# Kernel tuning notes

Measured on AMD Instinct MI355X. Metric: run time of the kernel, lower is better.

## Reference

```python
import jax, jax.numpy as jnp
import numpy as np

HEAD = 12
HEAD_DIM = 64  # dim // head = 768 // 12


def setup_inputs() -> dict:
    key = jax.random.key(0)
    k1, k2, k3 = jax.random.split(key, 3)
    B, N, D = 4, 2048, 768
    scale = 1.0 / np.sqrt(D)
    return {
        "x": jax.random.normal(k1, (B, N, D), dtype=jnp.float32),
        "w_qkv": jax.random.normal(k2, (D, 3 * D), dtype=jnp.float32) * scale,
        "w_proj": jax.random.normal(k3, (D, D), dtype=jnp.float32) * scale,
        "b_proj": jnp.zeros((D,), dtype=jnp.float32),
    }


def reference(x, w_qkv, w_proj, b_proj):
    B, N, D = x.shape
    qkv = x @ w_qkv  # [B, N, 3D]
    q, k, v = jnp.split(qkv, 3, axis=-1)
    # [B, H, N, k]
    def heads(t):
        return t.reshape(B, N, HEAD, HEAD_DIM).transpose(0, 2, 1, 3)
    q, k, v = heads(q), heads(k), heads(v)
    attn = jnp.einsum("bhnd,bhmd->bhnm", q, k) / jnp.sqrt(jnp.float32(HEAD_DIM))
    attn_prob = jax.nn.softmax(attn, axis=-1)  # dropout p=0.0 -> identity
    out = jnp.einsum("bhnm,bhmd->bhnd", attn_prob, v)
    out = out.transpose(0, 2, 1, 3).reshape(B, N, D)
    return out @ w_proj + b_proj
```

## Files before the change

### kernel.cpp

```cpp
#include <hip/hip_runtime.h>

typedef unsigned short u16;
typedef unsigned int u32;
typedef u16 u16x4 __attribute__((ext_vector_type(4)));
typedef u16 u16x8 __attribute__((ext_vector_type(8)));
typedef u32 u32x4 __attribute__((ext_vector_type(4)));
typedef __bf16 bf16x8 __attribute__((ext_vector_type(8)));
typedef float f32x4 __attribute__((ext_vector_type(4)));
typedef float f32x16 __attribute__((ext_vector_type(16)));

#define MFMA16 __builtin_amdgcn_mfma_f32_16x16x32_bf16
#define MFMA32 __builtin_amdgcn_mfma_f32_32x32x16_bf16

__device__ __forceinline__ u16 f2bf(float f) {
  return __builtin_bit_cast(u16, (__bf16)f);
}

__device__ __forceinline__ u32 pk2bf(float a, float b) {
  return (u32)__builtin_bit_cast(u16, (__bf16)a) |
         ((u32)__builtin_bit_cast(u16, (__bf16)b) << 16);
}

__device__ __forceinline__ void gload_lds16(const void* g, void* l) {
  __builtin_amdgcn_global_load_lds(
      (const __attribute__((address_space(1))) u32*)g,
      (__attribute__((address_space(3))) u32*)l, 16, 0, 0);
}

__global__ void cvt_f32_bf16_kernel(const float* __restrict__ in,
                                    u16* __restrict__ out, int n4) {
  int i = blockIdx.x * blockDim.x + threadIdx.x;
  if (i >= n4) return;
  float4 v = reinterpret_cast<const float4*>(in)[i];
  u16x4 o;
  o[0] = f2bf(v.x); o[1] = f2bf(v.y); o[2] = f2bf(v.z); o[3] = f2bf(v.w);
  reinterpret_cast<u16x4*>(out)[i] = o;
}

__global__ void transpose_cvt_kernel(const float* __restrict__ w,
                                     u16* __restrict__ wt, int K, int N) {
  __shared__ float t[32][33];
  int bk = blockIdx.x * 32, bn = blockIdx.y * 32;
  int x = threadIdx.x, y = threadIdx.y;
#pragma unroll
  for (int j = 0; j < 32; j += 8)
    t[y + j][x] = w[(size_t)(bk + y + j) * N + bn + x];
  __syncthreads();
#pragma unroll
  for (int j = 0; j < 32; j += 8)
    wt[(size_t)(bn + y + j) * K + bk + x] = f2bf(t[x][y + j]);
}

#define QSCALE 0.18033688011112042f

template <int NTOT, int EPI>
__global__ __launch_bounds__(256)
void gemm_bf16_kernel(const u16* __restrict__ A, const u16* __restrict__ BT,
                      u16* __restrict__ qo, u16* __restrict__ ko,
                      u16* __restrict__ vt, float* __restrict__ outF,
                      const float* __restrict__ bias) {
  __shared__ u16 sh[16384];
  u16* As = sh;
  u16* Bs = sh + 8192;
  const int tid = threadIdx.x;
  const int l = tid & 63, w = tid >> 6;
  const int lr = l & 15, lg = l >> 4;
  const int mtile = blockIdx.x & 63;
  const int ntile = blockIdx.x >> 6;
  const int mbase = mtile * 128, nbase = ntile * 128;
  const int wr = (w >> 1) * 64, wc = (w & 1) * 64;

  f32x4 acc[4][4] = {};

  for (int k0 = 0; k0 < 768; k0 += 64) {
#pragma unroll
    for (int i = 0; i < 4; ++i) {
      const int c = w * 64 + i * 256 + l;
      const int row = c >> 3, c16 = c & 7;
      const int sc = c16 ^ (row & 7);
      gload_lds16(A + (size_t)(mbase + row) * 768 + k0 + sc * 8,
                  &As[(size_t)(w * 64 + i * 256) * 8]);
      gload_lds16(BT + (size_t)(nbase + row) * 768 + k0 + sc * 8,
                  &Bs[(size_t)(w * 64 + i * 256) * 8]);
    }
    __syncthreads();
#pragma unroll
    for (int ks = 0; ks < 2; ++ks) {
      bf16x8 af[4], bfr[4];
#pragma unroll
      for (int m = 0; m < 4; ++m) {
        const int row = wr + m * 16 + lr;
        const int byte = (row * 128 + ks * 64 + lg * 16) ^ ((row & 7) << 4);
        af[m] = *reinterpret_cast<const bf16x8*>((const char*)As + byte);
      }
#pragma unroll
      for (int n = 0; n < 4; ++n) {
        const int row = wc + n * 16 + lr;
        const int byte = (row * 128 + ks * 64 + lg * 16) ^ ((row & 7) << 4);
        bfr[n] = *reinterpret_cast<const bf16x8*>((const char*)Bs + byte);
      }
#pragma unroll
      for (int m = 0; m < 4; ++m)
#pragma unroll
        for (int n = 0; n < 4; ++n)
          acc[m][n] = MFMA16(af[m], bfr[n], acc[m][n], 0, 0, 0);
    }
    __syncthreads();
  }

  if (EPI == 0 && ntile >= 12) {
    u16* vts = sh;
#pragma unroll
    for (int m = 0; m < 4; ++m)
#pragma unroll
      for (int n = 0; n < 4; ++n)
#pragma unroll
        for (int r = 0; r < 4; ++r) {
          const int col = wc + n * 16 + lr;
          const int row = wr + m * 16 + lg * 4 + r;
          const int byte = col * 256 + ((row * 2) ^ ((col & 7) << 4));
          *reinterpret_cast<u16*>((char*)vts + byte) = f2bf(acc[m][n][r]);
        }
    __syncthreads();
    const int b2 = mbase >> 11, nn0 = mbase & 2047;
#pragma unroll
    for (int i = 0; i < 8; ++i) {
      const int idx = i * 256 + tid;
      const int col = idx >> 4, u = idx & 15;
      u16x8 vv = *reinterpret_cast<u16x8*>(
          (char*)vts + (col * 256 + ((u * 16) ^ ((col & 7) << 4))));
      const int cg = nbase - 1536 + col;
      const int hh = cg >> 6, dd = cg & 63;
      *reinterpret_cast<u16x8*>(
          vt + (((size_t)(b2 * 12 + hh)) * 64 + dd) * 2048 + nn0 + u * 8) = vv;
    }
    return;
  }

#pragma unroll
  for (int m = 0; m < 4; ++m) {
#pragma unroll
    for (int n = 0; n < 4; ++n) {
#pragma unroll
      for (int r = 0; r < 4; ++r) {
        const int row = mbase + wr + m * 16 + lg * 4 + r;
        const int col = nbase + wc + n * 16 + lr;
        float val = acc[m][n][r];
        if (EPI == 0) {
          const int w2 = col / 768;
          const int c2 = col - w2 * 768;
          const int hh = c2 >> 6, dd = c2 & 63;
          const int b2 = row >> 11, nn = row & 2047;
          u16* dst = (w2 == 0) ? qo : ko;
          if (w2 == 0) val *= QSCALE;
          dst[(((size_t)(b2 * 12 + hh)) * 2048 + nn) * 64 + dd] = f2bf(val);
        } else {
          outF[(size_t)row * NTOT + col] = val + bias[col];
        }
      }
    }
  }
}

__global__ __launch_bounds__(256)
void flash_attn32_kernel(const u16* __restrict__ qb, const u16* __restrict__ kb,
                         const u16* __restrict__ vtb, u16* __restrict__ ao) {
  __shared__ u16 sh[16384];
  const int tid = threadIdx.x, w = tid >> 6, l = tid & 63;
  const int q5 = l & 31, hi = l >> 5;
  const int swz = (blockIdx.x & 7) * 96 + (blockIdx.x >> 3);
  const int bh = swz >> 4, qt = swz & 15;
  const int b = bh / 12, h = bh % 12;
  const int qrow0 = qt * 128 + w * 32;
  const u16* Q = qb + ((size_t)bh * 2048 + qrow0) * 64;
  const u16* K = kb + (size_t)bh * 2048 * 64;
  const u16* Vg = vtb + (size_t)bh * 64 * 2048;

  bf16x8 qf[4];
#pragma unroll
  for (int dk = 0; dk < 4; ++dk)
    qf[dk] = *reinterpret_cast<const bf16x8*>(Q + (size_t)q5 * 64 + dk * 16 + hi * 8);

  f32x16 ot0 = {}, ot1 = {};
  float l_ = 0.f;

  auto stage = [&](u16* base, int kt) {
#pragma unroll
    for (int i = 0; i < 2; ++i) {
      const int c = w * 64 + i * 256 + l;
      const int row = c >> 3, sc = (c & 7) ^ (row & 7);
      gload_lds16(K + (size_t)(kt + row) * 64 + sc * 8,
                  base + (size_t)(w * 64 + i * 256) * 8);
    }
#pragma unroll
    for (int i = 0; i < 2; ++i) {
      const int c = w * 64 + i * 256 + l;
      const int row = c >> 3, sc = (c & 7) ^ (row & 7);
      gload_lds16(Vg + (size_t)row * 2048 + kt + sc * 8,
                  base + 4096 + (size_t)(w * 64 + i * 256) * 8);
    }
  };

  stage(sh, 0);
  int cur = 0;
  const int swq = (q5 & 7) << 4;

  for (int kt = 0; kt < 2048; kt += 64) {
    u16* tb = sh + cur * 8192;
    __builtin_amdgcn_sched_barrier(0);
    __builtin_amdgcn_s_barrier();
    __builtin_amdgcn_sched_barrier(0);
    if (kt + 64 < 2048) {
      stage(sh + (cur ^ 1) * 8192, kt + 64);
      asm volatile("s_waitcnt vmcnt(4)" ::: "memory");
    } else {
      asm volatile("s_waitcnt vmcnt(0)" ::: "memory");
    }
    __builtin_amdgcn_sched_barrier(0);
    __builtin_amdgcn_s_barrier();
    __builtin_amdgcn_sched_barrier(0);

    const char* ksb = (const char*)tb;
    const char* vsb = (const char*)(tb + 4096);

    f32x16 st0 = {}, st1 = {};
    __builtin_amdgcn_s_setprio(1);
#pragma unroll
    for (int dk = 0; dk < 4; ++dk) {
      const int off = dk * 32 + hi * 16;
      bf16x8 kf0 = *reinterpret_cast<const bf16x8*>(ksb + ((q5 * 128 + off) ^ swq));
      bf16x8 kf1 = *reinterpret_cast<const bf16x8*>(ksb + (((q5 + 32) * 128 + off) ^ swq));
      st0 = MFMA32(kf0, qf[dk], st0, 0, 0, 0);
      st1 = MFMA32(kf1, qf[dk], st1, 0, 0, 0);
    }
    __builtin_amdgcn_s_setprio(0);

    float ls = 0.f;
#pragma unroll
    for (int r = 0; r < 16; ++r) {
      st0[r] = __builtin_amdgcn_exp2f(st0[r]); ls += st0[r];
    }
#pragma unroll
    for (int r = 0; r < 16; ++r) {
      st1[r] = __builtin_amdgcn_exp2f(st1[r]); ls += st1[r];
    }
    l_ += ls + __shfl_xor(ls, 32);

    __builtin_amdgcn_s_setprio(1);
#pragma unroll
    for (int kvs = 0; kvs < 4; ++kvs) {
      const f32x16& stx = (kvs < 2) ? st0 : st1;
      const int rb = (kvs & 1) * 8;
      const u32 A0 = pk2bf(stx[rb + 0], stx[rb + 1]);
      const u32 A1 = pk2bf(stx[rb + 2], stx[rb + 3]);
      const u32 A2 = pk2bf(stx[rb + 4], stx[rb + 5]);
      const u32 A3 = pk2bf(stx[rb + 6], stx[rb + 7]);
      const u32 s1 = hi ? A0 : A2, s2 = hi ? A1 : A3;
      const u32 r1 = (u32)__shfl_xor((int)s1, 32);
      const u32 r2 = (u32)__shfl_xor((int)s2, 32);
      u32x4 wv;
      wv[0] = hi ? r1 : A0; wv[1] = hi ? r2 : A1;
      wv[2] = hi ? A2 : r1; wv[3] = hi ? A3 : r2;
      const bf16x8 pf = __builtin_bit_cast(bf16x8, wv);
      const int off = kvs * 32 + hi * 16;
      bf16x8 vf0 = *reinterpret_cast<const bf16x8*>(vsb + ((q5 * 128 + off) ^ swq));
      bf16x8 vf1 = *reinterpret_cast<const bf16x8*>(vsb + (((q5 + 32) * 128 + off) ^ swq));
      ot0 = MFMA32(vf0, pf, ot0, 0, 0, 0);
      ot1 = MFMA32(vf1, pf, ot1, 0, 0, 0);
    }
    __builtin_amdgcn_s_setprio(0);
    cur ^= 1;
  }

  u16* ob = sh + w * 2048;
  const float inv = 1.0f / l_;
#pragma unroll
  for (int g = 0; g < 4; ++g) {
    u16x4 pk0, pk1;
#pragma unroll
    for (int r = 0; r < 4; ++r) {
      pk0[r] = f2bf(ot0[g * 4 + r] * inv);
      pk1[r] = f2bf(ot1[g * 4 + r] * inv);
    }
    const int d0 = hi * 4 + g * 8;
    *reinterpret_cast<u16x4*>((char*)ob + ((q5 * 128 + d0 * 2) ^ swq)) = pk0;
    *reinterpret_cast<u16x4*>((char*)ob + ((q5 * 128 + (d0 + 32) * 2) ^ swq)) = pk1;
  }
  __syncthreads();
#pragma unroll
  for (int i = 0; i < 4; ++i) {
    const int idx = i * 64 + l;
    const int qr = idx >> 3, cc = idx & 7;
    u16x8 vv = *reinterpret_cast<u16x8*>(
        (char*)ob + ((qr * 128 + cc * 16) ^ ((qr & 7) << 4)));
    *reinterpret_cast<u16x8*>(
        ao + ((size_t)(b * 2048 + qrow0 + qr)) * 768 + h * 64 + cc * 8) = vv;
  }
}

extern "C" void kernel_launch(void* const* d_in, const int* in_sizes, int n_in,
                              void* d_out, int out_size, void* d_ws,
                              size_t ws_size, hipStream_t stream) {
  const float* x = (const float*)d_in[0];
  const float* w_qkv = (const float*)d_in[1];
  const float* w_proj = (const float*)d_in[2];
  const float* b_proj = (const float*)d_in[3];
  float* out = (float*)d_out;

  char* ws = (char*)d_ws;
  size_t off = 0;
  auto alloc = [&](size_t bytes) {
    char* p = ws + off;
    off += (bytes + 255) & ~(size_t)255;
    return p;
  };
  u16* xb = (u16*)alloc(8192ull * 768 * 2);
  u16* wqkvT = (u16*)alloc(2304ull * 768 * 2);
  u16* wprojT = (u16*)alloc(768ull * 768 * 2);
  u16* qbuf = (u16*)alloc(48ull * 2048 * 64 * 2);
  u16* kbuf = (u16*)alloc(48ull * 2048 * 64 * 2);
  u16* vtb = (u16*)alloc(48ull * 64 * 2048 * 2);
  u16* aob = (u16*)alloc(8192ull * 768 * 2);
  (void)ws_size; (void)n_in; (void)in_sizes; (void)out_size;

  cvt_f32_bf16_kernel<<<(8192 * 768 / 4) / 256, 256, 0, stream>>>(
      x, xb, 8192 * 768 / 4);
  transpose_cvt_kernel<<<dim3(768 / 32, 2304 / 32), dim3(32, 8), 0, stream>>>(
      w_qkv, wqkvT, 768, 2304);
  transpose_cvt_kernel<<<dim3(768 / 32, 768 / 32), dim3(32, 8), 0, stream>>>(
      w_proj, wprojT, 768, 768);

  gemm_bf16_kernel<2304, 0><<<64 * 18, 256, 0, stream>>>(
      xb, wqkvT, qbuf, kbuf, vtb, nullptr, nullptr);

  flash_attn32_kernel<<<768, 256, 0, stream>>>(qbuf, kbuf, vtb, aob);

  gemm_bf16_kernel<768, 1><<<64 * 6, 256, 0, stream>>>(
      aob, wprojT, nullptr, nullptr, nullptr, out, b_proj);
}
```

Measured before the change: 164.3 us.

## Stage two KV tiles per barrier window and use permlane32 swap

The flash attention loop now loads two 64-key K/V tiles per pipeline stage into a doubled shared buffer, which halves the number of barrier pairs per block and deepens prefetch. The P-matrix lane exchange now uses the permlane32_swap builtin when it is available, in place of two ds_bpermute shuffles plus selects. The cost is double the LDS per block (64KB), which may lower occupancy.

Result: faster. 158.8 us (-3.3%).

```diff
diff --git a/kernel.cpp b/kernel.cpp
--- a/kernel.cpp
+++ b/kernel.cpp
@@ -4,6 +4,7 @@
 typedef unsigned int u32;
 typedef u16 u16x4 __attribute__((ext_vector_type(4)));
 typedef u16 u16x8 __attribute__((ext_vector_type(8)));
+typedef u32 u32x2 __attribute__((ext_vector_type(2)));
 typedef u32 u32x4 __attribute__((ext_vector_type(4)));
 typedef __bf16 bf16x8 __attribute__((ext_vector_type(8)));
 typedef float f32x4 __attribute__((ext_vector_type(4)));
@@ -19,6 +20,19 @@
 __device__ __forceinline__ u32 pk2bf(float a, float b) {
   return (u32)__builtin_bit_cast(u16, (__bf16)a) |
          ((u32)__builtin_bit_cast(u16, (__bf16)b) << 16);
+}
+
+__device__ __forceinline__ u32x2 swap32(u32 a, u32 b, int hi) {
+#if __has_builtin(__builtin_amdgcn_permlane32_swap)
+  (void)hi;
+  return __builtin_amdgcn_permlane32_swap(a, b, false, false);
+#else
+  u32 sa = (u32)__shfl_xor((int)a, 32), sb = (u32)__shfl_xor((int)b, 32);
+  u32x2 r;
+  r[0] = hi ? sb : a;
+  r[1] = hi ? b : sa;
+  return r;
+#endif
 }
 
 __device__ __forceinline__ void gload_lds16(const void* g, void* l) {
@@ -165,7 +179,7 @@
 __global__ __launch_bounds__(256)
 void flash_attn32_kernel(const u16* __restrict__ qb, const u16* __restrict__ kb,
                          const u16* __restrict__ vtb, u16* __restrict__ ao) {
-  __shared__ u16 sh[16384];
+  __shared__ u16 sh[32768];
   const int tid = threadIdx.x, w = tid >> 6, l = tid & 63;
   const int q5 = l & 31, hi = l >> 5;
   const int swz = (blockIdx.x & 7) * 96 + (blockIdx.x >> 3);
@@ -184,35 +198,40 @@
   f32x16 ot0 = {}, ot1 = {};
   float l_ = 0.f;
 
-  auto stage = [&](u16* base, int kt) {
-#pragma unroll
-    for (int i = 0; i < 2; ++i) {
-      const int c = w * 64 + i * 256 + l;
-      const int row = c >> 3, sc = (c & 7) ^ (row & 7);
-      gload_lds16(K + (size_t)(kt + row) * 64 + sc * 8,
-                  base + (size_t)(w * 64 + i * 256) * 8);
-    }
-#pragma unroll
-    for (int i = 0; i < 2; ++i) {
-      const int c = w * 64 + i * 256 + l;
-      const int row = c >> 3, sc = (c & 7) ^ (row & 7);
-      gload_lds16(Vg + (size_t)row * 2048 + kt + sc * 8,
-                  base + 4096 + (size_t)(w * 64 + i * 256) * 8);
+  auto stage2 = [&](u16* base, int kt0) {
+#pragma unroll
+    for (int s = 0; s < 2; ++s) {
+      u16* sb = base + s * 8192;
+      const int kt = kt0 + s * 64;
+#pragma unroll
+      for (int i = 0; i < 2; ++i) {
+        const int c = w * 64 + i * 256 + l;
+        const int row = c >> 3, sc = (c & 7) ^ (row & 7);
+        gload_lds16(K + (size_t)(kt + row) * 64 + sc * 8,
+                    sb + (size_t)(w * 64 + i * 256) * 8);
+      }
+#pragma unroll
+      for (int i = 0; i < 2; ++i) {
+        const int c = w * 64 + i * 256 + l;
+        const int row = c >> 3, sc = (c & 7) ^ (row & 7);
+        gload_lds16(Vg + (size_t)row * 2048 + kt + sc * 8,
+                    sb + 4096 + (size_t)(w * 64 + i * 256) * 8);
+      }
     }
   };
 
-  stage(sh, 0);
+  stage2(sh, 0);
   int cur = 0;
   const int swq = (q5 & 7) << 4;
 
-  for (int kt = 0; kt < 2048; kt += 64) {
-    u16* tb = sh + cur * 8192;
+  for (int win = 0; win < 16; ++win) {
+    u16* tb = sh + cur * 16384;
     __builtin_amdgcn_sched_barrier(0);
     __builtin_amdgcn_s_barrier();
     __builtin_amdgcn_sched_barrier(0);
-    if (kt + 64 < 2048) {
-      stage(sh + (cur ^ 1) * 8192, kt + 64);
-      asm volatile("s_waitcnt vmcnt(4)" ::: "memory");
+    if (win + 1 < 16) {
+      stage2(sh + (cur ^ 1) * 16384, (win + 1) * 128);
+      asm volatile("s_waitcnt vmcnt(8)" ::: "memory");
     } else {
       asm volatile("s_waitcnt vmcnt(0)" ::: "memory");
     }
@@ -220,55 +239,55 @@
     __builtin_amdgcn_s_barrier();
     __builtin_amdgcn_sched_barrier(0);
 
-    const char* ksb = (const char*)tb;
-    const char* vsb = (const char*)(tb + 4096);
-
-    f32x16 st0 = {}, st1 = {};
-    __builtin_amdgcn_s_setprio(1);
-#pragma unroll
-    for (int dk = 0; dk < 4; ++dk) {
-      const int off = dk * 32 + hi * 16;
-      bf16x8 kf0 = *reinterpret_cast<const bf16x8*>(ksb + ((q5 * 128 + off) ^ swq));
-      bf16x8 kf1 = *reinterpret_cast<const bf16x8*>(ksb + (((q5 + 32) * 128 + off) ^ swq));
-      st0 = MFMA32(kf0, qf[dk], st0, 0, 0, 0);
-      st1 = MFMA32(kf1, qf[dk], st1, 0, 0, 0);
-    }
-    __builtin_amdgcn_s_setprio(0);
-
-    float ls = 0.f;
-#pragma unroll
-    for (int r = 0; r < 16; ++r) {
-      st0[r] = __builtin_amdgcn_exp2f(st0[r]); ls += st0[r];
-    }
-#pragma unroll
-    for (int r = 0; r < 16; ++r) {
-      st1[r] = __builtin_amdgcn_exp2f(st1[r]); ls += st1[r];
-    }
-    l_ += ls + __shfl_xor(ls, 32);
-
-    __builtin_amdgcn_s_setprio(1);
-#pragma unroll
-    for (int kvs = 0; kvs < 4; ++kvs) {
-      const f32x16& stx = (kvs < 2) ? st0 : st1;
-      const int rb = (kvs & 1) * 8;
-      const u32 A0 = pk2bf(stx[rb + 0], stx[rb + 1]);
-      const u32 A1 = pk2bf(stx[rb + 2], stx[rb + 3]);
-      const u32 A2 = pk2bf(stx[rb + 4], stx[rb + 5]);
-      const u32 A3 = pk2bf(stx[rb + 6], stx[rb + 7]);
-      const u32 s1 = hi ? A0 : A2, s2 = hi ? A1 : A3;
-      const u32 r1 = (u32)__shfl_xor((int)s1, 32);
-      const u32 r2 = (u32)__shfl_xor((int)s2, 32);
-      u32x4 wv;
-      wv[0] = hi ? r1 : A0; wv[1] = hi ? r2 : A1;
-      wv[2] = hi ? A2 : r1; wv[3] = hi ? A3 : r2;
-      const bf16x8 pf = __builtin_bit_cast(bf16x8, wv);
-      const int off = kvs * 32 + hi * 16;
-      bf16x8 vf0 = *reinterpret_cast<const bf16x8*>(vsb + ((q5 * 128 + off) ^ swq));
-      bf16x8 vf1 = *reinterpret_cast<const bf16x8*>(vsb + (((q5 + 32) * 128 + off) ^ swq));
-      ot0 = MFMA32(vf0, pf, ot0, 0, 0, 0);
-      ot1 = MFMA32(vf1, pf, ot1, 0, 0, 0);
-    }
-    __builtin_amdgcn_s_setprio(0);
+    for (int s = 0; s < 2; ++s) {
+      const char* ksb = (const char*)(tb + s * 8192);
+      const char* vsb = (const char*)(tb + s * 8192 + 4096);
+
+      f32x16 st0 = {}, st1 = {};
+      __builtin_amdgcn_s_setprio(1);
+#pragma unroll
+      for (int dk = 0; dk < 4; ++dk) {
+        const int off = dk * 32 + hi * 16;
+        bf16x8 kf0 = *reinterpret_cast<const bf16x8*>(ksb + ((q5 * 128 + off) ^ swq));
+        bf16x8 kf1 = *reinterpret_cast<const bf16x8*>(ksb + (((q5 + 32) * 128 + off) ^ swq));
+        st0 = MFMA32(kf0, qf[dk], st0, 0, 0, 0);
+        st1 = MFMA32(kf1, qf[dk], st1, 0, 0, 0);
+      }
+      __builtin_amdgcn_s_setprio(0);
+
+      float ls = 0.f;
+#pragma unroll
+      for (int r = 0; r < 16; ++r) {
+        st0[r] = __builtin_amdgcn_exp2f(st0[r]); ls += st0[r];
+      }
+#pragma unroll
+      for (int r = 0; r < 16; ++r) {
+        st1[r] = __builtin_amdgcn_exp2f(st1[r]); ls += st1[r];
+      }
+      l_ += ls + __shfl_xor(ls, 32);
+
+      __builtin_amdgcn_s_setprio(1);
+#pragma unroll
+      for (int kvs = 0; kvs < 4; ++kvs) {
+        const f32x16& stx = (kvs < 2) ? st0 : st1;
+        const int rb = (kvs & 1) * 8;
+        const u32 A0 = pk2bf(stx[rb + 0], stx[rb + 1]);
+        const u32 A1 = pk2bf(stx[rb + 2], stx[rb + 3]);
+        const u32 A2 = pk2bf(stx[rb + 4], stx[rb + 5]);
+        const u32 A3 = pk2bf(stx[rb + 6], stx[rb + 7]);
+        const u32x2 p02 = swap32(A0, A2, hi);
+        const u32x2 p13 = swap32(A1, A3, hi);
+        u32x4 wv;
+        wv[0] = p02[0]; wv[1] = p13[0]; wv[2] = p02[1]; wv[3] = p13[1];
+        const bf16x8 pf = __builtin_bit_cast(bf16x8, wv);
+        const int off = kvs * 32 + hi * 16;
+        bf16x8 vf0 = *reinterpret_cast<const bf16x8*>(vsb + ((q5 * 128 + off) ^ swq));
+        bf16x8 vf1 = *reinterpret_cast<const bf16x8*>(vsb + (((q5 + 32) * 128 + off) ^ swq));
+        ot0 = MFMA32(vf0, pf, ot0, 0, 0, 0);
+        ot1 = MFMA32(vf1, pf, ot1, 0, 0, 0);
+      }
+      __builtin_amdgcn_s_setprio(0);
+    }
     cur ^= 1;
   }
 
```
